# Kernel tuning notes

Hardware: AMD Instinct MI355X
Metric: run time of the kernel (lower is better)

Reference implementation:

```python
import jax, jax.numpy as jnp
import numpy as np
import math

M = 0.65
S = 64.0
WEIGHT = 0.003
COS_M = math.cos(M)
SIN_M = math.sin(M)
THRESHOLD = math.cos(math.pi - M)
MM = math.sin(math.pi - M) * M

B, D, C = 512, 512, 100000


def l2_norm(x, axis):
    return x / jnp.linalg.norm(x, ord=2, axis=axis, keepdims=True)


def setup_inputs() -> dict:
    key = jax.random.key(0)
    k1, k2, k3 = jax.random.split(key, 3)
    embbedings = jax.random.normal(k1, (B, D), dtype=jnp.float32)
    kernel = 0.01 * jax.random.normal(k2, (D, C), dtype=jnp.float32)  # Parameter init std=0.01
    t = jnp.zeros((1,), dtype=jnp.float32)  # running buffer
    label = jax.random.randint(k3, (B,), 0, C, dtype=jnp.int64)
    return {"embbedings": embbedings, "kernel": kernel, "t": t, "label": label}


def reference(embbedings, kernel, t, label):
    emb = l2_norm(embbedings, axis=1)          # [B, D]
    kernel_norm = l2_norm(kernel, axis=0)      # [D, C]
    cos_theta = jnp.clip(emb @ kernel_norm, -1.0, 1.0)  # [B, C]
    origin_cos = jax.lax.stop_gradient(cos_theta)       # torch: clone under no_grad

    rows = jnp.arange(cos_theta.shape[0])
    target_logit = cos_theta[rows, label][:, None]       # [B, 1]
    sin_theta = jnp.sqrt(1.0 - target_logit ** 2)
    cos_theta_m = target_logit * COS_M - sin_theta * SIN_M

    mask = cos_theta > cos_theta_m                       # [B, C]
    final_target_logit = jnp.where(target_logit > THRESHOLD,
                                   cos_theta_m, target_logit - MM)

    # buffer update (no_grad), used immediately for hard-example reweighting
    t_new = jax.lax.stop_gradient(target_logit.mean()) * 0.01 + 0.99 * t  # [1]

    ct = jnp.where(mask, cos_theta * (t_new + cos_theta), cos_theta)
    ct = ct.at[rows, label].set(final_target_logit[:, 0])  # scatter_ on dim 1
    output = ct * S  # dropout with p=0 is identity

    # angular center loss; center is detached (no_grad clone) in torch
    center = jax.lax.stop_gradient(kernel.T)[label]       # [B, D]
    c_norm = l2_norm(center, axis=1)
    cos_theta_center = jnp.clip(jnp.sum(emb * c_norm, axis=1), -1.0, 1.0)
    center_loss = jnp.mean(jnp.arccos(cos_theta_center) ** 1.5)

    return output, origin_cos * S, S * WEIGHT * center_loss
```

## Files before the change

kernel.cpp:

```cpp
#include <hip/hip_runtime.h>
#include <hip/hip_bf16.h>
#include <stdint.h>

#define B_M 512
#define D_K 512
#define C_N 100000
#define S_SCALE 64.0f
#define W_LOSS 0.003f
#define COS_M_C 0.79608379854905604f
#define SIN_M_C 0.60518640573603957f
#define THRESH_C (-0.79608379854905604f)
#define MM_C 0.39337116372842573f

typedef __bf16 bf16x8 __attribute__((ext_vector_type(8)));
typedef float f32x4 __attribute__((ext_vector_type(4)));

typedef const __attribute__((address_space(1))) unsigned char* gptr_t;
typedef __attribute__((address_space(3))) unsigned char* sptr_t;

__device__ __forceinline__ unsigned short f2bf(float f) {
  __bf16 h = (__bf16)f;
  return __builtin_bit_cast(unsigned short, h);
}

__global__ __launch_bounds__(256) void prep_kernel(
    const float* __restrict__ emb, const float* __restrict__ Kg,
    const int* __restrict__ label, unsigned char* __restrict__ wsA,
    float* __restrict__ tl)
{
  int b = blockIdx.x, t = threadIdx.x;
  __shared__ float row[512];
  __shared__ float r1[256], r2[256];

  float2 v = ((const float2*)(emb + (size_t)b * 512))[t];
  r1[t] = v.x * v.x + v.y * v.y;
  __syncthreads();
  for (int s = 128; s > 0; s >>= 1) {
    if (t < s) r1[t] += r1[t + s];
    __syncthreads();
  }
  float inv = 1.0f / sqrtf(r1[0]);
  float e0 = v.x * inv, e1 = v.y * inv;
  row[2 * t] = e0;
  row[2 * t + 1] = e1;

  {
    int mhalf = b >> 8, lrow = b & 255;
    int kk = t >> 5;
    int byte_in = (4 * (t & 31)) ^ ((lrow & 7) << 4);
    ushort2 h;
    h.x = f2bf(e0);
    h.y = f2bf(e1);
    *(ushort2*)(wsA + (size_t)(mhalf * 8 + kk) * 32768 + lrow * 128 + byte_in) = h;
  }
  __syncthreads();

  int lab = label[b];
  const float* kc = Kg + lab;
  float dot = 0.f, csq = 0.f;
  for (int d = t; d < 512; d += 256) {
    float kv = kc[(size_t)d * C_N];
    dot += row[d] * kv;
    csq += kv * kv;
  }
  r1[t] = dot;
  r2[t] = csq;
  __syncthreads();
  for (int s = 128; s > 0; s >>= 1) {
    if (t < s) { r1[t] += r1[t + s]; r2[t] += r2[t + s]; }
    __syncthreads();
  }
  if (t == 0) {
    float tlv = r1[0] / sqrtf(r2[0]);
    tl[b] = fminf(1.f, fmaxf(-1.f, tlv));
  }
}

__global__ __launch_bounds__(512) void finalize_kernel(
    const float* __restrict__ tl, const float* __restrict__ t_in,
    float* __restrict__ ctm, float* __restrict__ ftl,
    float* __restrict__ tnew, float* __restrict__ out3)
{
  int t = threadIdx.x;
  float v = tl[t];
  __shared__ float r1[512], r2[512];
  float ac = acosf(v);
  r1[t] = v;
  r2[t] = ac * sqrtf(ac);
  __syncthreads();
  for (int s = 256; s > 0; s >>= 1) {
    if (t < s) { r1[t] += r1[t + s]; r2[t] += r2[t + s]; }
    __syncthreads();
  }
  if (t == 0) {
    tnew[0] = 0.99f * t_in[0] + 0.01f * (r1[0] / 512.0f);
    out3[0] = S_SCALE * W_LOSS * (r2[0] / 512.0f);
  }
  float st = sqrtf(fmaxf(0.f, 1.f - v * v));
  float cm = v * COS_M_C - st * SIN_M_C;
  ctm[t] = cm;
  ftl[t] = (v > THRESH_C) ? cm : (v - MM_C);
}

#define LDS_TOTAL 81920

__global__ __launch_bounds__(512, 2) void gemm_kernel(
    const float* __restrict__ Kg, const unsigned char* __restrict__ wsA,
    const float* __restrict__ ctm_g, const float* __restrict__ ftl_g,
    const int* __restrict__ label, const float* __restrict__ tnew_g,
    float* __restrict__ out1, float* __restrict__ out2)
{
  __shared__ __align__(16) unsigned char smem[LDS_TOTAL];

  int t = threadIdx.x;
  int lane = t & 63, wv = t >> 6;
  int wm = wv >> 2, wn = wv & 3;

  int bid = blockIdx.x;
  {
    const int q8 = 1564 / 8, r8 = 1564 % 8;
    int xcd = bid & 7, seq = bid >> 3;
    bid = (xcd < r8 ? xcd * (q8 + 1) : r8 * (q8 + 1) + (xcd - r8) * q8) + seq;
  }
  int pid = bid >> 1, mhalf = bid & 1;
  long c0 = (long)pid * 128;

  int c = t & 127, kseg = t >> 7;
  bool binb = (c0 + c) < C_N;
  const float* Bcol = Kg + c0 + c + (size_t)kseg * 16 * C_N;

  f32x4 acc[8][2] = {};
  float csq = 0.f;
  float bf0[16], bf1[16];

  const unsigned char* wsTile = wsA + (size_t)mhalf * (8 * 32768);
  unsigned char* smemB = smem + 65536;
  unsigned char* browB = smemB + c * 128;

#define LOAD_B(dst, j)                                                       \
  {                                                                          \
    const float* src = Bcol + (size_t)((j) * 64) * C_N;                      \
    _Pragma("unroll") for (int i = 0; i < 16; ++i)                           \
        dst[i] = binb ? src[(size_t)i * C_N] : 0.f;                          \
  }

#define WRITE_B(src)                                                         \
  {                                                                          \
    _Pragma("unroll") for (int i = 0; i < 16; ++i) csq += src[i] * src[i];   \
    union { unsigned short u[16]; uint4 q[2]; } pk;                          \
    _Pragma("unroll") for (int i = 0; i < 16; ++i) pk.u[i] = f2bf(src[i]);   \
    _Pragma("unroll") for (int h = 0; h < 2; ++h)                            \
      *(uint4*)(browB + ((kseg * 32 + h * 16) ^ ((c & 7) << 4))) = pk.q[h];  \
  }

  {
#pragma unroll
    for (int i = 0; i < 4; ++i) {
      int off = wv * 4096 + i * 1024;
      __builtin_amdgcn_global_load_lds((gptr_t)(wsTile + off + lane * 16),
                                       (sptr_t)(smem + off), 16, 0, 0);
    }
    __builtin_amdgcn_sched_barrier(0);
    LOAD_B(bf0, 0);
    __builtin_amdgcn_sched_barrier(0);
    LOAD_B(bf1, 1);
    __builtin_amdgcn_sched_barrier(0);
    asm volatile("s_waitcnt vmcnt(16)" ::: "memory");
    __builtin_amdgcn_sched_barrier(0);
    WRITE_B(bf0);
    __syncthreads();
  }

#pragma unroll
  for (int kkt = 0; kkt < 8; ++kkt) {
    int cur = kkt & 1;
    if (kkt < 7) {
      const unsigned char* tA = wsTile + (size_t)(kkt + 1) * 32768;
#pragma unroll
      for (int i = 0; i < 4; ++i) {
        int off = wv * 4096 + i * 1024;
        __builtin_amdgcn_global_load_lds((gptr_t)(tA + off + lane * 16),
                                         (sptr_t)(smem + (cur ^ 1) * 32768 + off), 16, 0, 0);
      }
      __builtin_amdgcn_sched_barrier(0);
    }
    if (kkt < 6) {
      if (kkt & 1) { LOAD_B(bf1, kkt + 2); } else { LOAD_B(bf0, kkt + 2); }
      __builtin_amdgcn_sched_barrier(0);
    }

    const unsigned char* Ab = smem + cur * 32768;
#pragma unroll
    for (int ks = 0; ks < 2; ++ks) {
      int kb = ks * 64 + (lane >> 4) * 16;
      bf16x8 bfr[2];
#pragma unroll
      for (int nf = 0; nf < 2; ++nf) {
        int n = wn * 32 + nf * 16 + (lane & 15);
        bfr[nf] = *(const bf16x8*)(smemB + n * 128 + (kb ^ ((n & 7) << 4)));
      }
#pragma unroll
      for (int mf = 0; mf < 8; ++mf) {
        int m = wm * 128 + mf * 16 + (lane & 15);
        bf16x8 afr = *(const bf16x8*)(Ab + m * 128 + (kb ^ ((m & 7) << 4)));
        acc[mf][0] = __builtin_amdgcn_mfma_f32_16x16x32_bf16(afr, bfr[0], acc[mf][0], 0, 0, 0);
        acc[mf][1] = __builtin_amdgcn_mfma_f32_16x16x32_bf16(afr, bfr[1], acc[mf][1], 0, 0, 0);
      }
    }

    if (kkt < 6) {
      asm volatile("s_waitcnt vmcnt(16)" ::: "memory");
    } else {
      asm volatile("s_waitcnt vmcnt(0)" ::: "memory");
    }
    __builtin_amdgcn_sched_barrier(0);
    __syncthreads();

    if (kkt < 7) {
      if (kkt & 1) { WRITE_B(bf0); } else { WRITE_B(bf1); }
      __syncthreads();
    }
  }

  float* colpart = (float*)(smemB);
  float* invn    = (float*)(smemB + 2048);
  float* ctm_s   = (float*)(smemB + 2560);
  float* ftl_s   = (float*)(smemB + 3584);
  int*   lab_s   = (int*)  (smemB + 4608);
  colpart[t] = csq;
  if (t < 256) {
    ctm_s[t] = ctm_g[mhalf * 256 + t];
    ftl_s[t] = ftl_g[mhalf * 256 + t];
    lab_s[t] = label[mhalf * 256 + t];
  }
  __syncthreads();
  if (t < 128) {
    float s = colpart[t] + colpart[128 + t] + colpart[256 + t] + colpart[384 + t];
    invn[t] = 1.0f / sqrtf(fmaxf(s, 1e-30f));
  }
  __syncthreads();
  float tn = tnew_g[0];

  for (int q = 0; q < 2; ++q) {
    if (wm == q) {
#pragma unroll
      for (int mf = 0; mf < 8; ++mf) {
#pragma unroll
        for (int nf = 0; nf < 2; ++nf) {
#pragma unroll
          for (int j = 0; j < 4; ++j) {
            int row = mf * 16 + (lane >> 4) * 4 + j;
            int col = wn * 32 + nf * 16 + (lane & 15);
            *(float*)(smem + row * 512 + ((col * 4) ^ (((row >> 2) & 3) << 6))) =
                acc[mf][nf][j];
          }
        }
      }
    }
    __syncthreads();
#pragma unroll
    for (int rr = 0; rr < 8; ++rr) {
      int row = rr * 16 + (t >> 5);
      int cb = (t & 31) * 4;
      f32x4 v = *(const f32x4*)(smem + row * 512 + ((cb * 4) ^ (((row >> 2) & 3) << 6)));
      long cgs = c0 + cb;
      if (cgs < C_N) {
        int lrow = q * 128 + row;
        float cm = ctm_s[lrow], fl = ftl_s[lrow];
        int lb = lab_s[lrow];
        f32x4 iv = *(const f32x4*)(invn + cb);
        f32x4 o1v, o2v;
#pragma unroll
        for (int jj = 0; jj < 4; ++jj) {
          float cosv = fminf(1.f, fmaxf(-1.f, v[jj] * iv[jj]));
          o2v[jj] = cosv * S_SCALE;
          float ct = (cosv > cm) ? cosv * (tn + cosv) : cosv;
          if (lb == (int)(cgs + jj)) ct = fl;
          o1v[jj] = ct * S_SCALE;
        }
        size_t idx = (size_t)(mhalf * 256 + lrow) * C_N + cgs;
        __builtin_nontemporal_store(o1v, (f32x4*)(out1 + idx));
        __builtin_nontemporal_store(o2v, (f32x4*)(out2 + idx));
      }
    }
    __syncthreads();
  }
#undef LOAD_B
#undef WRITE_B
}

extern "C" void kernel_launch(void* const* d_in, const int* in_sizes, int n_in,
                              void* d_out, int out_size, void* d_ws, size_t ws_size,
                              hipStream_t stream)
{
  const float* emb   = (const float*)d_in[0];
  const float* Kg    = (const float*)d_in[1];
  const float* t_in  = (const float*)d_in[2];
  const int*   label = (const int*)d_in[3];

  float* out1 = (float*)d_out;
  float* out2 = out1 + (size_t)B_M * C_N;
  float* out3 = out1 + 2 * (size_t)B_M * C_N;

  unsigned char* wsA = (unsigned char*)d_ws;
  float* tl   = (float*)((unsigned char*)d_ws + 524288);
  float* ctm  = tl + 512;
  float* ftl  = ctm + 512;
  float* tnew = ftl + 512;

  prep_kernel<<<512, 256, 0, stream>>>(emb, Kg, label, wsA, tl);
  finalize_kernel<<<1, 512, 0, stream>>>(tl, t_in, ctm, ftl, tnew, out3);
  int nb = 2 * ((C_N + 127) / 128);
  gemm_kernel<<<nb, 512, 0, stream>>>(Kg, wsA, ctm, ftl, label, tnew, out1, out2);
}
```

Baseline: 159.2 us.

## Fuse finalize into GEMM kernel and retile output to 100 columns per block

Removes the separate single-block finalize kernel. Every GEMM block now redundantly computes the 512-element mean and center-loss reduction and derives its own per-row margin values from the target logits. Only block 0 writes the loss scalar. It also changes the column tile so each block writes 100 of the 128 computed columns, which gives exactly 2000 blocks spread evenly over 8 XCDs and removes the ragged XCD remapping. In exchange, each block does extra MFMA work and B loads for 28 discarded columns, plus a redundant reduction.

```diff
diff --git a/kernel.cpp b/kernel.cpp
--- a/kernel.cpp
+++ b/kernel.cpp
@@ -5,6 +5,8 @@
 #define B_M 512
 #define D_K 512
 #define C_N 100000
+#define BN_OUT 100
+#define N_PID 1000
 #define S_SCALE 64.0f
 #define W_LOSS 0.003f
 #define COS_M_C 0.79608379854905604f
@@ -76,54 +78,29 @@
   }
 }
 
-__global__ __launch_bounds__(512) void finalize_kernel(
-    const float* __restrict__ tl, const float* __restrict__ t_in,
-    float* __restrict__ ctm, float* __restrict__ ftl,
-    float* __restrict__ tnew, float* __restrict__ out3)
-{
-  int t = threadIdx.x;
-  float v = tl[t];
-  __shared__ float r1[512], r2[512];
-  float ac = acosf(v);
-  r1[t] = v;
-  r2[t] = ac * sqrtf(ac);
-  __syncthreads();
-  for (int s = 256; s > 0; s >>= 1) {
-    if (t < s) { r1[t] += r1[t + s]; r2[t] += r2[t + s]; }
-    __syncthreads();
-  }
-  if (t == 0) {
-    tnew[0] = 0.99f * t_in[0] + 0.01f * (r1[0] / 512.0f);
-    out3[0] = S_SCALE * W_LOSS * (r2[0] / 512.0f);
-  }
-  float st = sqrtf(fmaxf(0.f, 1.f - v * v));
-  float cm = v * COS_M_C - st * SIN_M_C;
-  ctm[t] = cm;
-  ftl[t] = (v > THRESH_C) ? cm : (v - MM_C);
-}
-
 #define LDS_TOTAL 81920
 
 __global__ __launch_bounds__(512, 2) void gemm_kernel(
     const float* __restrict__ Kg, const unsigned char* __restrict__ wsA,
-    const float* __restrict__ ctm_g, const float* __restrict__ ftl_g,
-    const int* __restrict__ label, const float* __restrict__ tnew_g,
-    float* __restrict__ out1, float* __restrict__ out2)
+    const float* __restrict__ tl_g, const float* __restrict__ t_in_g,
+    const int* __restrict__ label,
+    float* __restrict__ out1, float* __restrict__ out2,
+    float* __restrict__ out3)
 {
   __shared__ __align__(16) unsigned char smem[LDS_TOTAL];
 
   int t = threadIdx.x;
   int lane = t & 63, wv = t >> 6;
   int wm = wv >> 2, wn = wv & 3;
+  bool orig0 = (blockIdx.x == 0);
 
   int bid = blockIdx.x;
   {
-    const int q8 = 1564 / 8, r8 = 1564 % 8;
     int xcd = bid & 7, seq = bid >> 3;
-    bid = (xcd < r8 ? xcd * (q8 + 1) : r8 * (q8 + 1) + (xcd - r8) * q8) + seq;
+    bid = xcd * 250 + seq;
   }
   int pid = bid >> 1, mhalf = bid & 1;
-  long c0 = (long)pid * 128;
+  long c0 = (long)pid * BN_OUT;
 
   int c = t & 127, kseg = t >> 7;
   bool binb = (c0 + c) < C_N;
@@ -222,24 +199,40 @@
     }
   }
 
-  float* colpart = (float*)(smemB);
-  float* invn    = (float*)(smemB + 2048);
-  float* ctm_s   = (float*)(smemB + 2560);
-  float* ftl_s   = (float*)(smemB + 3584);
-  int*   lab_s   = (int*)  (smemB + 4608);
+  float* red1    = (float*)(smemB);
+  float* red2    = (float*)(smemB + 2048);
+  float* colpart = (float*)(smemB + 4096);
+  float* invn    = (float*)(smemB + 6144);
+  float* ctm_s   = (float*)(smemB + 6656);
+  float* ftl_s   = (float*)(smemB + 7680);
+  int*   lab_s   = (int*)  (smemB + 8704);
+
+  float tlv = tl_g[t];
+  float acv = acosf(tlv);
+  red1[t] = tlv;
+  red2[t] = acv * sqrtf(acv);
   colpart[t] = csq;
-  if (t < 256) {
-    ctm_s[t] = ctm_g[mhalf * 256 + t];
-    ftl_s[t] = ftl_g[mhalf * 256 + t];
-    lab_s[t] = label[mhalf * 256 + t];
-  }
+  if (t < 256) lab_s[t] = label[mhalf * 256 + t];
   __syncthreads();
   if (t < 128) {
-    float s = colpart[t] + colpart[128 + t] + colpart[256 + t] + colpart[384 + t];
+    float s = colpart[t] + colpart[t + 128] + colpart[t + 256] + colpart[t + 384];
     invn[t] = 1.0f / sqrtf(fmaxf(s, 1e-30f));
-  }
-  __syncthreads();
-  float tn = tnew_g[0];
+  } else if (t >= 256) {
+    int r = t - 256;
+    float v2 = tl_g[mhalf * 256 + r];
+    float st = sqrtf(fmaxf(0.f, 1.f - v2 * v2));
+    float cm = v2 * COS_M_C - st * SIN_M_C;
+    ctm_s[r] = cm;
+    ftl_s[r] = (v2 > THRESH_C) ? cm : (v2 - MM_C);
+  }
+  for (int s = 256; s > 0; s >>= 1) {
+    __syncthreads();
+    if (t < s) { red1[t] += red1[t + s]; red2[t] += red2[t + s]; }
+  }
+  __syncthreads();
+  float tn = 0.99f * t_in_g[0] + 0.01f * (red1[0] * (1.0f / 512.0f));
+  if (orig0 && t == 0) out3[0] = S_SCALE * W_LOSS * (red2[0] * (1.0f / 512.0f));
+  __syncthreads();
 
   for (int q = 0; q < 2; ++q) {
     if (wm == q) {
@@ -263,8 +256,8 @@
       int row = rr * 16 + (t >> 5);
       int cb = (t & 31) * 4;
       f32x4 v = *(const f32x4*)(smem + row * 512 + ((cb * 4) ^ (((row >> 2) & 3) << 6)));
-      long cgs = c0 + cb;
-      if (cgs < C_N) {
+      if (cb < BN_OUT) {
+        long cgs = c0 + cb;
         int lrow = q * 128 + row;
         float cm = ctm_s[lrow], fl = ftl_s[lrow];
         int lb = lab_s[lrow];
@@ -303,13 +296,9 @@
   float* out3 = out1 + 2 * (size_t)B_M * C_N;
 
   unsigned char* wsA = (unsigned char*)d_ws;
-  float* tl   = (float*)((unsigned char*)d_ws + 524288);
-  float* ctm  = tl + 512;
-  float* ftl  = ctm + 512;
-  float* tnew = ftl + 512;
+  float* tl = (float*)((unsigned char*)d_ws + 524288);
 
   prep_kernel<<<512, 256, 0, stream>>>(emb, Kg, label, wsA, tl);
-  finalize_kernel<<<1, 512, 0, stream>>>(tl, t_in, ctm, ftl, tnew, out3);
-  int nb = 2 * ((C_N + 127) / 128);
-  gemm_kernel<<<nb, 512, 0, stream>>>(Kg, wsA, ctm, ftl, label, tnew, out1, out2);
+  gemm_kernel<<<2 * N_PID, 512, 0, stream>>>(Kg, wsA, tl, t_in, label,
+                                             out1, out2, out3);
 }
```

Result: slower. 209.0 us (+31.3%).
